# Kernel optimization log

Measured on AMD Instinct MI355X. Metric: run time of the kernel, lower is better.

## Reference

```python
import jax, jax.numpy as jnp
import numpy as np

HID = 64


def _rev_edges(row, col, n_nodes):
    # Find, for each directed edge (u,v), the index of its reverse (v,u).
    E = row.shape[0]
    keys = row.astype(jnp.int64) * n_nodes + col.astype(jnp.int64)
    rkeys = col.astype(jnp.int64) * n_nodes + row.astype(jnp.int64)
    order = jnp.argsort(keys)
    sk = keys[order]
    pos = jnp.clip(jnp.searchsorted(sk, rkeys), 0, E - 1)
    rev = order[pos]
    has_rev = sk[pos] == rkeys
    return rev, has_rev


def _dmpnn_conv(x, row, col, rev, has_rev, edge_hidden, Wm, bm, Wn, bn):
    # Original semantics: for edge i=(src,tgt), aggregate edge_hidden over all
    # edges j with row[j]==tgt, excluding the reverse edge (tgt,src).
    N = x.shape[0]
    seg = jax.ops.segment_sum(edge_hidden, row, num_segments=N)  # [N,H]
    msg_agg = seg[col] - jnp.where(has_rev[:, None], edge_hidden[rev], 0.0)  # [E,H]
    messages = jax.nn.relu(jnp.concatenate([x[row], msg_agg], axis=-1) @ Wm + bm)  # [E,H]
    node_msg = jax.ops.segment_sum(messages, col, num_segments=N)  # [N,H]
    x_out = jax.nn.relu(jnp.concatenate([x, node_msg], axis=-1) @ Wn + bn)  # [N,H]
    return x_out, messages


def setup_inputs() -> dict:
    key = jax.random.key(0)
    N, E2, B = 40000, 400000, 512  # nodes, undirected edges, graphs
    rng = np.random.default_rng(0)
    a = rng.integers(0, N, E2 * 3)
    b = rng.integers(0, N, E2 * 3)
    m = a != b
    a, b = a[m], b[m]
    canon = np.minimum(a, b).astype(np.int64) * N + np.maximum(a, b)
    _, uidx = np.unique(canon, return_index=True)
    uidx = np.sort(uidx)[:E2]
    a, b = a[uidx], b[uidx]
    row = np.concatenate([a, b]).astype(np.int32)
    col = np.concatenate([b, a]).astype(np.int32)
    edge_index = jnp.asarray(np.stack([row, col]))  # [2, 2*E2], every edge has a reverse
    E = edge_index.shape[1]
    batch = jnp.sort(jax.random.randint(jax.random.fold_in(key, 1), (N,), 0, B, dtype=jnp.int32))
    ks = jax.random.split(jax.random.fold_in(key, 2), 26)
    nrm = lambda k, s: jax.random.normal(k, s, dtype=jnp.float32)
    p = lambda k, s: nrm(k, s) * 0.05
    return {
        "x": nrm(ks[0], (N, 78)),
        "edge_attr": nrm(ks[1], (E, 6)),
        "xt": nrm(ks[2], (B, 128)),
        "edge_index": edge_index,
        "batch": batch,
        "n_graphs": B,
        "We": p(ks[3], (6, HID)), "be": p(ks[4], (HID,)),
        "Wm1": p(ks[5], (78 + HID, HID)), "bm1": p(ks[6], (HID,)),
        "Wn1": p(ks[7], (78 + HID, HID)), "bn1": p(ks[8], (HID,)),
        "Wm2": p(ks[9], (2 * HID, HID)), "bm2": p(ks[10], (HID,)),
        "Wn2": p(ks[11], (2 * HID, HID)), "bn2": p(ks[12], (HID,)),
        "Wm3": p(ks[13], (2 * HID, HID)), "bm3": p(ks[14], (HID,)),
        "Wn3": p(ks[15], (2 * HID, HID)), "bn3": p(ks[16], (HID,)),
        "Wxd": p(ks[17], (HID, 128)), "bxd": p(ks[18], (128,)),
        "W1": p(ks[19], (256, 1024)), "b1": p(ks[20], (1024,)),
        "W2": p(ks[21], (1024, 256)), "b2": p(ks[22], (256,)),
        "Wo": p(ks[23], (256, 1)), "bo": p(ks[24], (1,)),
    }


def reference(x, edge_attr, xt, edge_index, batch, n_graphs, We, be, Wm1, bm1, Wn1, bn1, Wm2, bm2, Wn2, bn2, Wm3, bm3, Wn3, bn3, Wxd, bxd, W1, b1, W2, b2, Wo, bo):
    N = x.shape[0]
    row, col = edge_index[0], edge_index[1]
    rev, has_rev = _rev_edges(row, col, N)
    eh = edge_attr @ We + be  # edge_init
    x1, eh = _dmpnn_conv(x, row, col, rev, has_rev, eh, Wm1, bm1, Wn1, bn1)
    x2, eh = _dmpnn_conv(x1, row, col, rev, has_rev, eh, Wm2, bm2, Wn2, bn2)
    x3, eh = _dmpnn_conv(x2, row, col, rev, has_rev, eh, Wm3, bm3, Wn3, bn3)
    pooled = jax.ops.segment_sum(x3, batch, num_segments=n_graphs)  # global_add_pool
    xg = jax.nn.relu(pooled @ Wxd + bxd)  # [B,128]
    xc = jnp.concatenate([xg, xt], axis=1)  # [B,256]
    h = jax.nn.relu(xc @ W1 + b1)
    h = jax.nn.relu(h @ W2 + b2)
    return h @ Wo + bo  # [B,1]
```

## Files before the change

### kernel.cpp

```cpp
#include <hip/hip_runtime.h>
#include <hip/hip_bf16.h>

using u16 = unsigned short;
using u32 = unsigned int;
using u64 = unsigned long long;

typedef short short8 __attribute__((ext_vector_type(8)));
typedef float f32x4 __attribute__((ext_vector_type(4)));

#define WP_TOP   0
#define WP_BOT   6144
#define WP_NTOP  10240
#define WP_NBOT  16384
#define WP_LAYER 20480

__device__ __forceinline__ float bf2f(u32 u){ union{u32 i; float f;} v; v.i = u<<16; return v.f; }
__device__ __forceinline__ u32 f2bf(float f){ union{float f; u32 i;} v; v.f=f; u32 i=v.i; return (i + 0x7FFFu + ((i>>16)&1u)) >> 16; }
__device__ __forceinline__ u32 pack2(float a, float b){ return f2bf(a) | (f2bf(b)<<16); }

__device__ __forceinline__ void store16bf(u16* d, const float* a){
  uint4 u0, u1;
  u0.x = pack2(a[0],a[1]);   u0.y = pack2(a[2],a[3]);
  u0.z = pack2(a[4],a[5]);   u0.w = pack2(a[6],a[7]);
  u1.x = pack2(a[8],a[9]);   u1.y = pack2(a[10],a[11]);
  u1.z = pack2(a[12],a[13]); u1.w = pack2(a[14],a[15]);
  *(uint4*)(d)   = u0;
  *(uint4*)(d+8) = u1;
}

__global__ __launch_bounds__(256) void k_deg(
    const int* __restrict__ row, int* __restrict__ cnt, int E)
{
  int e = blockIdx.x*256 + threadIdx.x;
  if (e >= E) return;
  atomicAdd(&cnt[row[e]], 1);
}

__global__ __launch_bounds__(256) void k_bsum(
    const int* __restrict__ cnt, int* __restrict__ bsum, int N)
{
  __shared__ int sh[256];
  int t = threadIdx.x;
  int i = blockIdx.x*256 + t;
  sh[t] = (i < N) ? cnt[i] : 0;
  __syncthreads();
  #pragma unroll
  for (int s=128; s; s>>=1){ if (t<s) sh[t]+=sh[t+s]; __syncthreads(); }
  if (t==0) bsum[blockIdx.x] = sh[0];
}

__global__ __launch_bounds__(256) void k_bscan(
    const int* __restrict__ bsum, int* __restrict__ bofs, int nb,
    int* __restrict__ off, int N)
{
  __shared__ int sh[256];
  int t = threadIdx.x;
  int v = (t < nb) ? bsum[t] : 0;
  sh[t] = v;
  __syncthreads();
  #pragma unroll
  for (int s=1; s<256; s<<=1){
    int u = (t>=s) ? sh[t-s] : 0;
    __syncthreads();
    sh[t] += u;
    __syncthreads();
  }
  if (t < nb) bofs[t] = sh[t] - v;
  if (t == 0) off[N] = sh[nb-1];
}

__global__ __launch_bounds__(256) void k_apply(
    const int* __restrict__ cnt, const int* __restrict__ bofs,
    int* __restrict__ off, int* __restrict__ nxt, int N)
{
  __shared__ int sh[256];
  int t = threadIdx.x;
  int i = blockIdx.x*256 + t;
  int v = (i < N) ? cnt[i] : 0;
  sh[t] = v;
  __syncthreads();
  #pragma unroll
  for (int s=1; s<256; s<<=1){
    int u = (t>=s) ? sh[t-s] : 0;
    __syncthreads();
    sh[t] += u;
    __syncthreads();
  }
  if (i < N){
    int ex = sh[t] - v + bofs[blockIdx.x];
    off[i] = ex;
    nxt[i] = ex;
  }
}

__global__ __launch_bounds__(256) void k_fill(
    const int* __restrict__ row, int* __restrict__ nxt,
    int* __restrict__ perm, int* __restrict__ iperm, int E)
{
  int e = blockIdx.x*256 + threadIdx.x;
  if (e >= E) return;
  int pos = atomicAdd(&nxt[row[e]], 1);
  perm[pos] = e;
  iperm[e] = pos;
}

__global__ __launch_bounds__(256) void k_permarr(
    const int* __restrict__ perm, const int* __restrict__ iperm,
    const int* __restrict__ row, const int* __restrict__ col,
    int* __restrict__ rowp, int* __restrict__ colp, int* __restrict__ revp,
    int E, int E2)
{
  int i = blockIdx.x*256 + threadIdx.x;
  if (i >= E) return;
  int e = perm[i];
  rowp[i] = row[e];
  colp[i] = col[e];
  int re = (e < E2) ? e + E2 : e - E2;
  revp[i] = iperm[re];
}

__global__ __launch_bounds__(256) void k_xconv(
    const float* __restrict__ x, u16* __restrict__ xbf, int N)
{
  int t = blockIdx.x*256 + threadIdx.x;
  if (t >= N*96) return;
  int n = t / 96, k = t - n*96;
  xbf[t] = (k < 78) ? (u16)f2bf(x[(size_t)n*78 + k]) : (u16)0;
}

__global__ __launch_bounds__(256) void k_edge_init(
    const float* __restrict__ ea, const int* __restrict__ perm,
    const float* __restrict__ We, const float* __restrict__ be,
    u16* __restrict__ eh, int E)
{
  int tid = blockIdx.x*256 + threadIdx.x;
  int i = tid >> 2;
  if (i >= E) return;
  int t = tid & 3;
  int e = perm[i];
  const float* a = ea + (size_t)e*6;
  float acc[16];
  #pragma unroll
  for (int j=0;j<16;j++) acc[j] = be[t*16+j];
  #pragma unroll
  for (int k=0;k<6;k++){
    float av = a[k];
    const float* w = We + k*64 + t*16;
    #pragma unroll
    for (int j=0;j<16;j++) acc[j] += av*w[j];
  }
  store16bf(eh + ((size_t)i<<6) + t*16, acc);
}

__global__ __launch_bounds__(256) void k_prepw(
    const float* __restrict__ Wm, const float* __restrict__ Wn,
    int XD, int KT, u16* __restrict__ dst)
{
  int t = blockIdx.x*256 + threadIdx.x;
  int topFL = KT*256;
  const float* W; int rbase, rvalid, dofs, fl;
  if (t < topFL)                   { W = Wm; rbase = 0;  rvalid = XD; dofs = WP_TOP;  fl = t; }
  else if (t < topFL+512)          { W = Wm; rbase = XD; rvalid = 64; dofs = WP_BOT;  fl = t - topFL; }
  else if (t < 2*topFL+512)        { W = Wn; rbase = 0;  rvalid = XD; dofs = WP_NTOP; fl = t - topFL - 512; }
  else if (t < 2*topFL+1024)       { W = Wn; rbase = XD; rvalid = 64; dofs = WP_NBOT; fl = t - 2*topFL - 512; }
  else return;
  int f = fl >> 6, lane = fl & 63;
  int nt = f & 3, kk = f >> 2;
  int n = (nt<<4) + (lane & 15);
  int krel = (kk<<5) + ((lane>>4)<<3);
  u16* d = dst + dofs + (size_t)f*512 + lane*8;
  #pragma unroll
  for (int j=0;j<8;j++){
    int kr = krel + j;
    d[j] = (kr < rvalid) ? (u16)f2bf(W[(size_t)(rbase+kr)*64 + n]) : (u16)0;
  }
}

__global__ __launch_bounds__(256) void k_packw(
    const float* __restrict__ W, int K, int Nout, u16* __restrict__ dst)
{
  int t = blockIdx.x*256 + threadIdx.x;
  int NT = Nout >> 4;
  int total = (K >> 5) * NT * 64;
  if (t >= total) return;
  int f = t >> 6, lane = t & 63;
  int nt = f % NT, kk = f / NT;
  int n = (nt<<4) + (lane & 15);
  int kb = (kk<<5) + ((lane>>4)<<3);
  u16* d = dst + ((size_t)f*64 + lane)*8;
  #pragma unroll
  for (int j=0;j<8;j++) d[j] = (u16)f2bf(W[(size_t)(kb+j)*Nout + n]);
}

__global__ __launch_bounds__(256) void k_gemm(
    const u16* __restrict__ A, int lda, const u16* __restrict__ BP,
    const float* __restrict__ bias, void* __restrict__ outv, int ldo,
    int M, int NT, int KT, int dorelu, int obf16)
{
  int lane = threadIdx.x & 63;
  int wid = (blockIdx.x << 2) + (threadIdx.x >> 6);
  int nb = NT >> 2;
  int mblk = wid / nb, nblk = wid - mblk*nb;
  int m0 = mblk << 4;
  if (m0 >= M) return;
  int n0 = nblk << 6;
  int nlo = lane & 15;
  int khi = (lane >> 4) << 3;
  int r0 = m0 + nlo; if (r0 > M-1) r0 = M-1;

  f32x4 acc[4];
  #pragma unroll
  for (int nt=0;nt<4;nt++){ f32x4 z = {0.f,0.f,0.f,0.f}; acc[nt]=z; }
  for (int kk=0; kk<KT; kk++){
    short8 a = *(const short8*)(A + (size_t)r0*lda + (kk<<5) + khi);
    #pragma unroll
    for (int nt=0;nt<4;nt++){
      short8 b = *(const short8*)(BP + ((size_t)(kk*NT + (nblk<<2) + nt)*64 + lane)*8);
      acc[nt] = __builtin_amdgcn_mfma_f32_16x16x32_bf16(a, b, acc[nt], 0,0,0);
    }
  }
  int mrow = (lane >> 4) << 2;
  #pragma unroll
  for (int r=0;r<4;r++){
    int m = m0 + mrow + r;
    if (m >= M) continue;
    #pragma unroll
    for (int nt=0;nt<4;nt++){
      float v = acc[nt][r] + bias[n0 + (nt<<4) + nlo];
      if (dorelu) v = fmaxf(v, 0.f);
      if (obf16) ((u16*)outv)[(size_t)m*ldo + n0 + (nt<<4) + nlo] = (u16)f2bf(v);
      else       ((float*)outv)[(size_t)m*ldo + n0 + (nt<<4) + nlo] = v;
    }
  }
}

__global__ __launch_bounds__(256) void k_seg(
    const u16* __restrict__ eh, const int* __restrict__ off,
    u16* __restrict__ segb, int N)
{
  int w = (blockIdx.x << 2) + (threadIdx.x >> 6);
  if (w >= N) return;
  int lane = threadIdx.x & 63;
  int lo = off[w], hi = off[w+1];
  float s = 0.f;
  for (int i = lo; i < hi; i++) s += bf2f((u32)eh[((size_t)i<<6) + lane]);
  segb[((size_t)w<<6) + lane] = (u16)f2bf(s);
}

template<int KT>
__global__ __launch_bounds__(256) void k_proj(
    const u16* __restrict__ xin, const u16* __restrict__ segb,
    const u16* __restrict__ wp, const float* __restrict__ bm,
    u16* __restrict__ pxb, u16* __restrict__ psb, int N)
{
  int lane = threadIdx.x & 63;
  int wid = (blockIdx.x << 2) + (threadIdx.x >> 6);
  int base = wid << 4;
  if (base >= N) return;
  int nlo = lane & 15;
  int khi = (lane >> 4) << 3;

  short8 bt[KT][4];
  #pragma unroll
  for (int kk=0;kk<KT;kk++)
    #pragma unroll
    for (int nt=0;nt<4;nt++)
      bt[kk][nt] = *(const short8*)(wp + WP_TOP + ((size_t)((kk<<2)|nt)*64 + lane)*8);
  short8 bb[2][4];
  #pragma unroll
  for (int kk=0;kk<2;kk++)
    #pragma unroll
    for (int nt=0;nt<4;nt++)
      bb[kk][nt] = *(const short8*)(wp + WP_BOT + ((size_t)((kk<<2)|nt)*64 + lane)*8);

  int r0 = base + nlo; if (r0 > N-1) r0 = N-1;
  const u16* xrow = xin + (size_t)r0*(KT*32);
  short8 ax[KT];
  #pragma unroll
  for (int kk=0;kk<KT;kk++) ax[kk] = *(const short8*)(xrow + (kk<<5) + khi);
  const u16* srow = segb + ((size_t)r0<<6);
  short8 as[2];
  #pragma unroll
  for (int kk=0;kk<2;kk++) as[kk] = *(const short8*)(srow + (kk<<5) + khi);

  f32x4 accP[4], accS[4];
  #pragma unroll
  for (int nt=0;nt<4;nt++){ f32x4 z = {0.f,0.f,0.f,0.f}; accP[nt]=z; accS[nt]=z; }
  #pragma unroll
  for (int kk=0;kk<KT;kk++)
    #pragma unroll
    for (int nt=0;nt<4;nt++)
      accP[nt] = __builtin_amdgcn_mfma_f32_16x16x32_bf16(ax[kk], bt[kk][nt], accP[nt], 0,0,0);
  #pragma unroll
  for (int kk=0;kk<2;kk++)
    #pragma unroll
    for (int nt=0;nt<4;nt++)
      accS[nt] = __builtin_amdgcn_mfma_f32_16x16x32_bf16(as[kk], bb[kk][nt], accS[nt], 0,0,0);

  float bmv[4];
  #pragma unroll
  for (int nt=0;nt<4;nt++) bmv[nt] = bm[(nt<<4) + nlo];

  int mrow = (lane >> 4) << 2;
  #pragma unroll
  for (int r=0;r<4;r++){
    int node = base + mrow + r;
    if (node >= N) continue;
    #pragma unroll
    for (int nt=0;nt<4;nt++){
      pxb[((size_t)node<<6) + (nt<<4) + nlo] = (u16)f2bf(accP[nt][r] + bmv[nt]);
      psb[((size_t)node<<6) + (nt<<4) + nlo] = (u16)f2bf(accS[nt][r]);
    }
  }
}

__global__ __launch_bounds__(256) void k_scatmfma(
    const u16* __restrict__ eh, const u16* __restrict__ wp,
    const u16* __restrict__ pxb, const u16* __restrict__ psb,
    const int* __restrict__ rowp, const int* __restrict__ colp,
    const int* __restrict__ revp, u16* __restrict__ msg, int E)
{
  int lane = threadIdx.x & 63;
  int wid = (blockIdx.x << 2) + (threadIdx.x >> 6);
  int base = wid << 4;
  if (base >= E) return;
  int nlo = lane & 15;
  int khi = (lane >> 4) << 3;

  short8 bb[2][4];
  #pragma unroll
  for (int kk=0;kk<2;kk++)
    #pragma unroll
    for (int nt=0;nt<4;nt++)
      bb[kk][nt] = *(const short8*)(wp + WP_BOT + ((size_t)((kk<<2)|nt)*64 + lane)*8);

  int sa = base + nlo; if (sa > E-1) sa = E-1;
  const u16* ehp = eh + ((size_t)sa<<6) + khi;
  short8 a0 = *(const short8*)(ehp);
  short8 a1 = *(const short8*)(ehp + 32);

  f32x4 acc[4];
  #pragma unroll
  for (int nt=0;nt<4;nt++){
    f32x4 z = {0.f,0.f,0.f,0.f};
    acc[nt] = z;
    acc[nt] = __builtin_amdgcn_mfma_f32_16x16x32_bf16(a0, bb[0][nt], acc[nt], 0,0,0);
    acc[nt] = __builtin_amdgcn_mfma_f32_16x16x32_bf16(a1, bb[1][nt], acc[nt], 0,0,0);
  }

  int mrow = (lane >> 4) << 2;
  #pragma unroll
  for (int r=0;r<4;r++){
    int slot = base + mrow + r;
    if (slot >= E) continue;
    int rp = rowp[slot];
    int cp = colp[slot];
    int rv = revp[slot];
    const u16* pr = psb + ((size_t)rp<<6) + nlo;
    const u16* pc = pxb + ((size_t)cp<<6) + nlo;
    u16* ob = msg + ((size_t)rv<<6) + nlo;
    #pragma unroll
    for (int nt=0;nt<4;nt++){
      float v = bf2f((u32)pc[nt<<4]) + bf2f((u32)pr[nt<<4]) - acc[nt][r];
      ob[nt<<4] = (u16)f2bf(fmaxf(v, 0.f));
    }
  }
}

__global__ __launch_bounds__(256) void k_gnmsg(
    const u16* __restrict__ msg, const int* __restrict__ revp,
    const int* __restrict__ off, u16* __restrict__ nmsgb,
    u16* __restrict__ segnext, int N)
{
  int w = (blockIdx.x << 2) + (threadIdx.x >> 6);
  if (w >= N) return;
  int lane = threadIdx.x & 63;
  int lo = off[w], hi = off[w+1];
  float s = 0.f, sg = 0.f;
  if (segnext) {
    for (int j = lo; j < hi; j++) {
      int i = revp[j];
      s  += bf2f((u32)msg[((size_t)i<<6) + lane]);
      sg += bf2f((u32)msg[((size_t)j<<6) + lane]);
    }
    segnext[((size_t)w<<6) + lane] = (u16)f2bf(sg);
  } else {
    for (int j = lo; j < hi; j++) {
      int i = revp[j];
      s += bf2f((u32)msg[((size_t)i<<6) + lane]);
    }
  }
  nmsgb[((size_t)w<<6) + lane] = (u16)f2bf(s);
}

template<int KT>
__global__ __launch_bounds__(256) void k_nodef(
    const u16* __restrict__ xin, const u16* __restrict__ nmsgb,
    const u16* __restrict__ wp, const float* __restrict__ bn,
    u16* __restrict__ xout, int N)
{
  int lane = threadIdx.x & 63;
  int wid = (blockIdx.x << 2) + (threadIdx.x >> 6);
  int base = wid << 4;
  if (base >= N) return;
  int nlo = lane & 15;
  int khi = (lane >> 4) << 3;

  short8 bt[KT][4];
  #pragma unroll
  for (int kk=0;kk<KT;kk++)
    #pragma unroll
    for (int nt=0;nt<4;nt++)
      bt[kk][nt] = *(const short8*)(wp + WP_NTOP + ((size_t)((kk<<2)|nt)*64 + lane)*8);
  short8 bb[2][4];
  #pragma unroll
  for (int kk=0;kk<2;kk++)
    #pragma unroll
    for (int nt=0;nt<4;nt++)
      bb[kk][nt] = *(const short8*)(wp + WP_NBOT + ((size_t)((kk<<2)|nt)*64 + lane)*8);

  int r0 = base + nlo; if (r0 > N-1) r0 = N-1;
  const u16* xrow = xin + (size_t)r0*(KT*32);
  short8 ax[KT];
  #pragma unroll
  for (int kk=0;kk<KT;kk++) ax[kk] = *(const short8*)(xrow + (kk<<5) + khi);
  const u16* mrp = nmsgb + ((size_t)r0<<6);
  short8 am[2];
  #pragma unroll
  for (int kk=0;kk<2;kk++) am[kk] = *(const short8*)(mrp + (kk<<5) + khi);

  f32x4 acc[4];
  #pragma unroll
  for (int nt=0;nt<4;nt++){ f32x4 z = {0.f,0.f,0.f,0.f}; acc[nt]=z; }
  #pragma unroll
  for (int kk=0;kk<KT;kk++)
    #pragma unroll
    for (int nt=0;nt<4;nt++)
      acc[nt] = __builtin_amdgcn_mfma_f32_16x16x32_bf16(ax[kk], bt[kk][nt], acc[nt], 0,0,0);
  #pragma unroll
  for (int kk=0;kk<2;kk++)
    #pragma unroll
    for (int nt=0;nt<4;nt++)
      acc[nt] = __builtin_amdgcn_mfma_f32_16x16x32_bf16(am[kk], bb[kk][nt], acc[nt], 0,0,0);

  float bnv[4];
  #pragma unroll
  for (int nt=0;nt<4;nt++) bnv[nt] = bn[(nt<<4) + nlo];

  int mrow = (lane >> 4) << 2;
  #pragma unroll
  for (int r=0;r<4;r++){
    int node = base + mrow + r;
    if (node >= N) continue;
    #pragma unroll
    for (int nt=0;nt<4;nt++)
      xout[((size_t)node<<6) + (nt<<4) + nlo] = (u16)f2bf(fmaxf(acc[nt][r] + bnv[nt], 0.f));
  }
}

__global__ __launch_bounds__(256) void k_goff(
    const int* __restrict__ batch, int* __restrict__ goff, int N, int B)
{
  int n = blockIdx.x*256 + threadIdx.x;
  if (n >= N) return;
  int bcur = batch[n];
  int bprev = (n == 0) ? -1 : batch[n-1];
  for (int g = bprev + 1; g <= bcur; ++g) goff[g] = n;
  if (n == N-1) { for (int g = bcur + 1; g <= B; ++g) goff[g] = N; }
}

__global__ __launch_bounds__(256) void k_pool(
    const u16* __restrict__ xin, const int* __restrict__ goff,
    u16* __restrict__ pooledb, int B)
{
  int g = (blockIdx.x << 2) + (threadIdx.x >> 6);
  if (g >= B) return;
  int lane = threadIdx.x & 63;
  int lo = goff[g], hi = goff[g + 1];
  float s = 0.f;
  for (int n = lo; n < hi; n++) s += bf2f((u32)xin[((size_t)n << 6) + lane]);
  pooledb[((size_t)g << 6) + lane] = (u16)f2bf(s);
}

__global__ __launch_bounds__(256) void k_xtconv(
    const float* __restrict__ xt, u16* __restrict__ ab1, int B)
{
  int t = blockIdx.x*256 + threadIdx.x;
  if (t >= B*128) return;
  int r = t >> 7, c = t & 127;
  ab1[(size_t)r*256 + 128 + c] = (u16)f2bf(xt[t]);
}

__global__ __launch_bounds__(256) void k_out(
    const float* __restrict__ h2, const float* __restrict__ Wo,
    const float* __restrict__ bo, float* __restrict__ out, int B)
{
  int w = (blockIdx.x << 2) + (threadIdx.x >> 6);
  if (w >= B) return;
  int lane = threadIdx.x & 63;
  const float* h = h2 + (size_t)w*256;
  float s = 0.f;
  #pragma unroll
  for (int k=0;k<4;k++) s += h[lane + (k<<6)] * Wo[lane + (k<<6)];
  #pragma unroll
  for (int off=32; off; off>>=1) s += __shfl_down(s, off, 64);
  if (lane == 0) out[w] = s + bo[0];
}

extern "C" void kernel_launch(void* const* d_in, const int* in_sizes, int n_in,
                              void* d_out, int out_size, void* d_ws, size_t ws_size,
                              hipStream_t stream)
{
  const float* x    = (const float*)d_in[0];
  const float* ea   = (const float*)d_in[1];
  const float* xt   = (const float*)d_in[2];
  const int*   eidx = (const int*)d_in[3];
  const int*   batch= (const int*)d_in[4];
  const float* We   = (const float*)d_in[6];
  const float* be   = (const float*)d_in[7];
  const float* Wm[3]= {(const float*)d_in[8],  (const float*)d_in[12], (const float*)d_in[16]};
  const float* bm[3]= {(const float*)d_in[9],  (const float*)d_in[13], (const float*)d_in[17]};
  const float* Wn[3]= {(const float*)d_in[10], (const float*)d_in[14], (const float*)d_in[18]};
  const float* bn[3]= {(const float*)d_in[11], (const float*)d_in[15], (const float*)d_in[19]};
  const float* Wxd  = (const float*)d_in[20];
  const float* bxd  = (const float*)d_in[21];
  const float* W1   = (const float*)d_in[22];
  const float* b1   = (const float*)d_in[23];
  const float* W2   = (const float*)d_in[24];
  const float* b2   = (const float*)d_in[25];
  const float* Wo   = (const float*)d_in[26];
  const float* bo   = (const float*)d_in[27];

  const int N = in_sizes[0] / 78;
  const int E = in_sizes[1] / 6;
  const int B = in_sizes[2] / 128;
  const int E2 = E / 2;
  const int* row = eidx;
  const int* col = eidx + E;

  char* p = (char*)d_ws;
  size_t off = 0;
  auto alloc = [&](size_t b)->void* {
    void* r = p + off;
    off = (off + b + 255) & ~(size_t)255;
    return r;
  };
  u16*   ehA   = (u16*)  alloc((size_t)E * 128);
  u16*   ehB   = (u16*)  alloc((size_t)E * 128);
  int*   rowp  = (int*)  alloc((size_t)E * 4);
  int*   colp  = (int*)  alloc((size_t)E * 4);
  int*   revp  = (int*)  alloc((size_t)E * 4);
  int*   offs  = (int*)  alloc((size_t)(N+1) * 4);
  u16*   xbf   = (u16*)  alloc((size_t)N * 192);
  u16*   sA    = (u16*)  alloc((size_t)N * 128);
  u16*   sB    = (u16*)  alloc((size_t)N * 128);
  u16*   pxb   = (u16*)  alloc((size_t)N * 128);
  u16*   psb   = (u16*)  alloc((size_t)N * 128);
  u16*   xa    = (u16*)  alloc((size_t)N * 128);
  u16*   xb    = (u16*)  alloc((size_t)N * 128);
  int*   goff  = (int*)  alloc((size_t)(B+1) * 4);
  u16*   pooledb=(u16*)  alloc((size_t)B * 128);
  u16*   ab1   = (u16*)  alloc((size_t)B * 512);
  u16*   h1b   = (u16*)  alloc((size_t)B * 2048);
  float* h2f   = (float*)alloc((size_t)B * 1024);
  u16*   wpack = (u16*)  alloc((size_t)3 * WP_LAYER * 2);
  u16*   wxdP  = (u16*)  alloc((size_t)(64/32)*(128/16)*512 * 2);
  u16*   w1P   = (u16*)  alloc((size_t)(256/32)*(1024/16)*512 * 2);
  u16*   w2P   = (u16*)  alloc((size_t)(1024/32)*(256/16)*512 * 2);

  char* ehBc = (char*)ehB;
  int* perm  = (int*)ehBc;
  int* iperm = perm + E;
  int* cnt   = iperm + E;
  int* nxt   = cnt + N;
  int* bsum  = nxt + N;
  int* bofs  = bsum + 1024;

  dim3 blk(256);
  int gE   = (E + 255) / 256;
  int gE4  = ((size_t)E*4 + 255) / 256;
  int gEm  = (E + 63) / 64;
  int gN   = (N + 255) / 256;
  int gNm  = (N + 63) / 64;
  int gNw  = (N + 3) / 4;
  int gBw  = (B + 3) / 4;
  int gXc  = (N*96 + 255) / 256;
  int nb   = (N + 255) / 256;

  hipMemsetAsync(cnt, 0, (size_t)N * 4, stream);
  k_deg  <<<gE, blk, 0, stream>>>(row, cnt, E);
  k_bsum <<<nb, blk, 0, stream>>>(cnt, bsum, N);
  k_bscan<<<1,  blk, 0, stream>>>(bsum, bofs, nb, offs, N);
  k_apply<<<nb, blk, 0, stream>>>(cnt, bofs, offs, nxt, N);
  k_fill <<<gE, blk, 0, stream>>>(row, nxt, perm, iperm, E);
  k_permarr<<<gE, blk, 0, stream>>>(perm, iperm, row, col, rowp, colp, revp, E, E2);
  k_edge_init<<<gE4, blk, 0, stream>>>(ea, perm, We, be, ehA, E);
  k_xconv<<<gXc, blk, 0, stream>>>(x, xbf, N);
  k_goff<<<gN, blk, 0, stream>>>(batch, goff, N, B);
  for (int L = 0; L < 3; ++L) {
    int XD = (L == 0) ? 78 : 64;
    int KT = (L == 0) ? 3 : 2;
    k_prepw<<<10, blk, 0, stream>>>(Wm[L], Wn[L], XD, KT, wpack + (size_t)L*WP_LAYER);
  }
  k_packw<<<(1024 + 255)/256, blk, 0, stream>>>(Wxd, 64, 128, wxdP);
  k_packw<<<(32768 + 255)/256, blk, 0, stream>>>(W1, 256, 1024, w1P);
  k_packw<<<(32768 + 255)/256, blk, 0, stream>>>(W2, 1024, 256, w2P);

  k_seg<<<gNw, blk, 0, stream>>>(ehA, offs, sA, N);

  const u16* ehin = ehA;
  u16* ehout = ehB;
  const u16* xin = xbf;
  u16* segcur = sA;
  u16* segnxt = sB;
  for (int L = 0; L < 3; ++L) {
    u16* xout = (L % 2 == 0) ? xa : xb;
    const u16* wp = wpack + (size_t)L*WP_LAYER;
    if (L == 0) k_proj<3><<<gNm, blk, 0, stream>>>(xin, segcur, wp, bm[L], pxb, psb, N);
    else        k_proj<2><<<gNm, blk, 0, stream>>>(xin, segcur, wp, bm[L], pxb, psb, N);
    k_scatmfma<<<gEm, blk, 0, stream>>>(ehin, wp, pxb, psb, rowp, colp, revp, ehout, E);
    k_gnmsg<<<gNw, blk, 0, stream>>>(ehout, revp, offs, pxb, (L < 2) ? segnxt : (u16*)nullptr, N);
    if (L == 0) k_nodef<3><<<gNm, blk, 0, stream>>>(xin, pxb, wp, bn[L], xout, N);
    else        k_nodef<2><<<gNm, blk, 0, stream>>>(xin, pxb, wp, bn[L], xout, N);
    u16* tmp = (u16*)ehin; ehin = ehout; ehout = tmp;
    u16* ts = segcur; segcur = segnxt; segnxt = ts;
    xin = xout;
  }

  k_pool<<<gBw, blk, 0, stream>>>(xa, goff, pooledb, B);
  k_xtconv<<<(B*128 + 255)/256, blk, 0, stream>>>(xt, ab1, B);
  {
    int waves = ((B + 15)/16) * (128/64);
    k_gemm<<<(waves + 3)/4, blk, 0, stream>>>(pooledb, 64, wxdP, bxd, ab1, 256, B, 128>>4, 64>>5, 1, 1);
  }
  {
    int waves = ((B + 15)/16) * (1024/64);
    k_gemm<<<(waves + 3)/4, blk, 0, stream>>>(ab1, 256, w1P, b1, h1b, 1024, B, 1024>>4, 256>>5, 1, 1);
  }
  {
    int waves = ((B + 15)/16) * (256/64);
    k_gemm<<<(waves + 3)/4, blk, 0, stream>>>(h1b, 1024, w2P, b2, h2f, 256, B, 256>>4, 1024>>5, 1, 0);
  }
  k_out<<<gBw, blk, 0, stream>>>(h2f, Wo, bo, (float*)d_out, B);
}
```

Measured before the change: 815.4 us.

## Switch to fp16, fold edge-init into first segment sum, vectorize gather

Moves all 16-bit storage and MFMA from bf16 to fp16, trading exponent range for cheaper hardware conversions and more mantissa. The edge-init kernel now iterates in original edge order and scatters into sorted slots. The first segment sum is computed algebraically from raw 6-wide edge attributes rather than re-reading the 64-wide hidden state. The per-node message gather uses four edge groups per wave with 8-byte loads and shuffle reductions to expose more memory parallelism.

```diff
diff --git a/kernel.cpp b/kernel.cpp
--- a/kernel.cpp
+++ b/kernel.cpp
@@ -1,5 +1,5 @@
 #include <hip/hip_runtime.h>
-#include <hip/hip_bf16.h>
+#include <hip/hip_fp16.h>
 
 using u16 = unsigned short;
 using u32 = unsigned int;
@@ -14,11 +14,11 @@
 #define WP_NBOT  16384
 #define WP_LAYER 20480
 
-__device__ __forceinline__ float bf2f(u32 u){ union{u32 i; float f;} v; v.i = u<<16; return v.f; }
-__device__ __forceinline__ u32 f2bf(float f){ union{float f; u32 i;} v; v.f=f; u32 i=v.i; return (i + 0x7FFFu + ((i>>16)&1u)) >> 16; }
-__device__ __forceinline__ u32 pack2(float a, float b){ return f2bf(a) | (f2bf(b)<<16); }
-
-__device__ __forceinline__ void store16bf(u16* d, const float* a){
+__device__ __forceinline__ float h2f(u16 u){ union{u16 s; _Float16 h;} v; v.s=u; return (float)v.h; }
+__device__ __forceinline__ u16 f2h(float f){ union{u16 s; _Float16 h;} v; v.h=(_Float16)f; return v.s; }
+__device__ __forceinline__ u32 pack2(float a, float b){ return (u32)f2h(a) | ((u32)f2h(b)<<16); }
+
+__device__ __forceinline__ void store16h(u16* d, const float* a){
   uint4 u0, u1;
   u0.x = pack2(a[0],a[1]);   u0.y = pack2(a[2],a[3]);
   u0.z = pack2(a[4],a[5]);   u0.w = pack2(a[6],a[7]);
@@ -120,24 +120,24 @@
 }
 
 __global__ __launch_bounds__(256) void k_xconv(
-    const float* __restrict__ x, u16* __restrict__ xbf, int N)
+    const float* __restrict__ x, u16* __restrict__ xh, int N)
 {
   int t = blockIdx.x*256 + threadIdx.x;
   if (t >= N*96) return;
   int n = t / 96, k = t - n*96;
-  xbf[t] = (k < 78) ? (u16)f2bf(x[(size_t)n*78 + k]) : (u16)0;
+  xh[t] = (k < 78) ? f2h(x[(size_t)n*78 + k]) : (u16)0;
 }
 
 __global__ __launch_bounds__(256) void k_edge_init(
-    const float* __restrict__ ea, const int* __restrict__ perm,
+    const float* __restrict__ ea, const int* __restrict__ iperm,
     const float* __restrict__ We, const float* __restrict__ be,
     u16* __restrict__ eh, int E)
 {
   int tid = blockIdx.x*256 + threadIdx.x;
-  int i = tid >> 2;
-  if (i >= E) return;
+  int e = tid >> 2;
+  if (e >= E) return;
   int t = tid & 3;
-  int e = perm[i];
+  int slot = iperm[e];
   const float* a = ea + (size_t)e*6;
   float acc[16];
   #pragma unroll
@@ -149,7 +149,32 @@
     #pragma unroll
     for (int j=0;j<16;j++) acc[j] += av*w[j];
   }
-  store16bf(eh + ((size_t)i<<6) + t*16, acc);
+  store16h(eh + ((size_t)slot<<6) + t*16, acc);
+}
+
+__global__ __launch_bounds__(256) void k_seg0(
+    const float* __restrict__ ea, const int* __restrict__ perm,
+    const int* __restrict__ off, const float* __restrict__ We,
+    const float* __restrict__ be, u16* __restrict__ segb, int N)
+{
+  int w = (blockIdx.x << 2) + (threadIdx.x >> 6);
+  if (w >= N) return;
+  int lane = threadIdx.x & 63;
+  int lo = off[w], hi = off[w+1];
+  float wcol[6];
+  #pragma unroll
+  for (int k=0;k<6;k++) wcol[k] = We[k*64 + lane];
+  float es[6] = {0.f,0.f,0.f,0.f,0.f,0.f};
+  for (int j = lo; j < hi; j++){
+    int e = perm[j];
+    const float* a = ea + (size_t)e*6;
+    #pragma unroll
+    for (int k=0;k<6;k++) es[k] += a[k];
+  }
+  float acc = (float)(hi - lo) * be[lane];
+  #pragma unroll
+  for (int k=0;k<6;k++) acc += es[k]*wcol[k];
+  segb[((size_t)w<<6) + lane] = f2h(acc);
 }
 
 __global__ __launch_bounds__(256) void k_prepw(
@@ -172,7 +197,7 @@
   #pragma unroll
   for (int j=0;j<8;j++){
     int kr = krel + j;
-    d[j] = (kr < rvalid) ? (u16)f2bf(W[(size_t)(rbase+kr)*64 + n]) : (u16)0;
+    d[j] = (kr < rvalid) ? f2h(W[(size_t)(rbase+kr)*64 + n]) : (u16)0;
   }
 }
 
@@ -189,13 +214,13 @@
   int kb = (kk<<5) + ((lane>>4)<<3);
   u16* d = dst + ((size_t)f*64 + lane)*8;
   #pragma unroll
-  for (int j=0;j<8;j++) d[j] = (u16)f2bf(W[(size_t)(kb+j)*Nout + n]);
+  for (int j=0;j<8;j++) d[j] = f2h(W[(size_t)(kb+j)*Nout + n]);
 }
 
 __global__ __launch_bounds__(256) void k_gemm(
     const u16* __restrict__ A, int lda, const u16* __restrict__ BP,
     const float* __restrict__ bias, void* __restrict__ outv, int ldo,
-    int M, int NT, int KT, int dorelu, int obf16)
+    int M, int NT, int KT, int dorelu, int oh16)
 {
   int lane = threadIdx.x & 63;
   int wid = (blockIdx.x << 2) + (threadIdx.x >> 6);
@@ -216,7 +241,7 @@
     #pragma unroll
     for (int nt=0;nt<4;nt++){
       short8 b = *(const short8*)(BP + ((size_t)(kk*NT + (nblk<<2) + nt)*64 + lane)*8);
-      acc[nt] = __builtin_amdgcn_mfma_f32_16x16x32_bf16(a, b, acc[nt], 0,0,0);
+      acc[nt] = __builtin_amdgcn_mfma_f32_16x16x32_f16(a, b, acc[nt], 0,0,0);
     }
   }
   int mrow = (lane >> 4) << 2;
@@ -228,23 +253,10 @@
     for (int nt=0;nt<4;nt++){
       float v = acc[nt][r] + bias[n0 + (nt<<4) + nlo];
       if (dorelu) v = fmaxf(v, 0.f);
-      if (obf16) ((u16*)outv)[(size_t)m*ldo + n0 + (nt<<4) + nlo] = (u16)f2bf(v);
-      else       ((float*)outv)[(size_t)m*ldo + n0 + (nt<<4) + nlo] = v;
+      if (oh16) ((u16*)outv)[(size_t)m*ldo + n0 + (nt<<4) + nlo] = f2h(v);
+      else      ((float*)outv)[(size_t)m*ldo + n0 + (nt<<4) + nlo] = v;
     }
   }
-}
-
-__global__ __launch_bounds__(256) void k_seg(
-    const u16* __restrict__ eh, const int* __restrict__ off,
-    u16* __restrict__ segb, int N)
-{
-  int w = (blockIdx.x << 2) + (threadIdx.x >> 6);
-  if (w >= N) return;
-  int lane = threadIdx.x & 63;
-  int lo = off[w], hi = off[w+1];
-  float s = 0.f;
-  for (int i = lo; i < hi; i++) s += bf2f((u32)eh[((size_t)i<<6) + lane]);
-  segb[((size_t)w<<6) + lane] = (u16)f2bf(s);
 }
 
 template<int KT>
@@ -290,12 +302,12 @@
   for (int kk=0;kk<KT;kk++)
     #pragma unroll
     for (int nt=0;nt<4;nt++)
-      accP[nt] = __builtin_amdgcn_mfma_f32_16x16x32_bf16(ax[kk], bt[kk][nt], accP[nt], 0,0,0);
+      accP[nt] = __builtin_amdgcn_mfma_f32_16x16x32_f16(ax[kk], bt[kk][nt], accP[nt], 0,0,0);
   #pragma unroll
   for (int kk=0;kk<2;kk++)
     #pragma unroll
     for (int nt=0;nt<4;nt++)
-      accS[nt] = __builtin_amdgcn_mfma_f32_16x16x32_bf16(as[kk], bb[kk][nt], accS[nt], 0,0,0);
+      accS[nt] = __builtin_amdgcn_mfma_f32_16x16x32_f16(as[kk], bb[kk][nt], accS[nt], 0,0,0);
 
   float bmv[4];
   #pragma unroll
@@ -308,8 +320,8 @@
     if (node >= N) continue;
     #pragma unroll
     for (int nt=0;nt<4;nt++){
-      pxb[((size_t)node<<6) + (nt<<4) + nlo] = (u16)f2bf(accP[nt][r] + bmv[nt]);
-      psb[((size_t)node<<6) + (nt<<4) + nlo] = (u16)f2bf(accS[nt][r]);
+      pxb[((size_t)node<<6) + (nt<<4) + nlo] = f2h(accP[nt][r] + bmv[nt]);
+      psb[((size_t)node<<6) + (nt<<4) + nlo] = f2h(accS[nt][r]);
     }
   }
 }
@@ -344,8 +356,8 @@
   for (int nt=0;nt<4;nt++){
     f32x4 z = {0.f,0.f,0.f,0.f};
     acc[nt] = z;
-    acc[nt] = __builtin_amdgcn_mfma_f32_16x16x32_bf16(a0, bb[0][nt], acc[nt], 0,0,0);
-    acc[nt] = __builtin_amdgcn_mfma_f32_16x16x32_bf16(a1, bb[1][nt], acc[nt], 0,0,0);
+    acc[nt] = __builtin_amdgcn_mfma_f32_16x16x32_f16(a0, bb[0][nt], acc[nt], 0,0,0);
+    acc[nt] = __builtin_amdgcn_mfma_f32_16x16x32_f16(a1, bb[1][nt], acc[nt], 0,0,0);
   }
 
   int mrow = (lane >> 4) << 2;
@@ -361,8 +373,8 @@
     u16* ob = msg + ((size_t)rv<<6) + nlo;
     #pragma unroll
     for (int nt=0;nt<4;nt++){
-      float v = bf2f((u32)pc[nt<<4]) + bf2f((u32)pr[nt<<4]) - acc[nt][r];
-      ob[nt<<4] = (u16)f2bf(fmaxf(v, 0.f));
+      float v = h2f(pc[nt<<4]) + h2f(pr[nt<<4]) - acc[nt][r];
+      ob[nt<<4] = f2h(fmaxf(v, 0.f));
     }
   }
 }
@@ -375,22 +387,43 @@
   int w = (blockIdx.x << 2) + (threadIdx.x >> 6);
   if (w >= N) return;
   int lane = threadIdx.x & 63;
+  int g = lane >> 4, l = lane & 15;
   int lo = off[w], hi = off[w+1];
-  float s = 0.f, sg = 0.f;
-  if (segnext) {
-    for (int j = lo; j < hi; j++) {
+  float s0=0.f,s1=0.f,s2=0.f,s3=0.f;
+  float t0=0.f,t1=0.f,t2=0.f,t3=0.f;
+  if (segnext){
+    for (int j = lo + g; j < hi; j += 4){
       int i = revp[j];
-      s  += bf2f((u32)msg[((size_t)i<<6) + lane]);
-      sg += bf2f((u32)msg[((size_t)j<<6) + lane]);
+      uint2 v = *(const uint2*)(msg + ((size_t)i<<6) + (l<<2));
+      uint2 u = *(const uint2*)(msg + ((size_t)j<<6) + (l<<2));
+      s0 += h2f((u16)v.x); s1 += h2f((u16)(v.x>>16)); s2 += h2f((u16)v.y); s3 += h2f((u16)(v.y>>16));
+      t0 += h2f((u16)u.x); t1 += h2f((u16)(u.x>>16)); t2 += h2f((u16)u.y); t3 += h2f((u16)(u.y>>16));
     }
-    segnext[((size_t)w<<6) + lane] = (u16)f2bf(sg);
   } else {
-    for (int j = lo; j < hi; j++) {
+    for (int j = lo + g; j < hi; j += 4){
       int i = revp[j];
-      s += bf2f((u32)msg[((size_t)i<<6) + lane]);
+      uint2 v = *(const uint2*)(msg + ((size_t)i<<6) + (l<<2));
+      s0 += h2f((u16)v.x); s1 += h2f((u16)(v.x>>16)); s2 += h2f((u16)v.y); s3 += h2f((u16)(v.y>>16));
     }
   }
-  nmsgb[((size_t)w<<6) + lane] = (u16)f2bf(s);
+  s0 += __shfl_xor(s0,16,64); s0 += __shfl_xor(s0,32,64);
+  s1 += __shfl_xor(s1,16,64); s1 += __shfl_xor(s1,32,64);
+  s2 += __shfl_xor(s2,16,64); s2 += __shfl_xor(s2,32,64);
+  s3 += __shfl_xor(s3,16,64); s3 += __shfl_xor(s3,32,64);
+  if (segnext){
+    t0 += __shfl_xor(t0,16,64); t0 += __shfl_xor(t0,32,64);
+    t1 += __shfl_xor(t1,16,64); t1 += __shfl_xor(t1,32,64);
+    t2 += __shfl_xor(t2,16,64); t2 += __shfl_xor(t2,32,64);
+    t3 += __shfl_xor(t3,16,64); t3 += __shfl_xor(t3,32,64);
+  }
+  if (g == 0){
+    uint2 o; o.x = pack2(s0,s1); o.y = pack2(s2,s3);
+    *(uint2*)(nmsgb + ((size_t)w<<6) + (l<<2)) = o;
+    if (segnext){
+      uint2 q; q.x = pack2(t0,t1); q.y = pack2(t2,t3);
+      *(uint2*)(segnext + ((size_t)w<<6) + (l<<2)) = q;
+    }
+  }
 }
 
 template<int KT>
@@ -436,12 +469,12 @@
   for (int kk=0;kk<KT;kk++)
     #pragma unroll
     for (int nt=0;nt<4;nt++)
-      acc[nt] = __builtin_amdgcn_mfma_f32_16x16x32_bf16(ax[kk], bt[kk][nt], acc[nt], 0,0,0);
+      acc[nt] = __builtin_amdgcn_mfma_f32_16x16x32_f16(ax[kk], bt[kk][nt], acc[nt], 0,0,0);
   #pragma unroll
   for (int kk=0;kk<2;kk++)
     #pragma unroll
     for (int nt=0;nt<4;nt++)
-      acc[nt] = __builtin_amdgcn_mfma_f32_16x16x32_bf16(am[kk], bb[kk][nt], acc[nt], 0,0,0);
+      acc[nt] = __builtin_amdgcn_mfma_f32_16x16x32_f16(am[kk], bb[kk][nt], acc[nt], 0,0,0);
 
   float bnv[4];
   #pragma unroll
@@ -454,7 +487,7 @@
     if (node >= N) continue;
     #pragma unroll
     for (int nt=0;nt<4;nt++)
-      xout[((size_t)node<<6) + (nt<<4) + nlo] = (u16)f2bf(fmaxf(acc[nt][r] + bnv[nt], 0.f));
+      xout[((size_t)node<<6) + (nt<<4) + nlo] = f2h(fmaxf(acc[nt][r] + bnv[nt], 0.f));
   }
 }
 
@@ -471,15 +504,15 @@
 
 __global__ __launch_bounds__(256) void k_pool(
     const u16* __restrict__ xin, const int* __restrict__ goff,
-    u16* __restrict__ pooledb, int B)
+    u16* __restrict__ pooledh, int B)
 {
   int g = (blockIdx.x << 2) + (threadIdx.x >> 6);
   if (g >= B) return;
   int lane = threadIdx.x & 63;
   int lo = goff[g], hi = goff[g + 1];
   float s = 0.f;
-  for (int n = lo; n < hi; n++) s += bf2f((u32)xin[((size_t)n << 6) + lane]);
-  pooledb[((size_t)g << 6) + lane] = (u16)f2bf(s);
+  for (int n = lo; n < hi; n++) s += h2f(xin[((size_t)n << 6) + lane]);
+  pooledh[((size_t)g << 6) + lane] = f2h(s);
 }
 
 __global__ __launch_bounds__(256) void k_xtconv(
@@ -488,7 +521,7 @@
   int t = blockIdx.x*256 + threadIdx.x;
   if (t >= B*128) return;
   int r = t >> 7, c = t & 127;
-  ab1[(size_t)r*256 + 128 + c] = (u16)f2bf(xt[t]);
+  ab1[(size_t)r*256 + 128 + c] = f2h(xt[t]);
 }
 
 __global__ __launch_bounds__(256) void k_out(
@@ -551,7 +584,7 @@
   int*   colp  = (int*)  alloc((size_t)E * 4);
   int*   revp  = (int*)  alloc((size_t)E * 4);
   int*   offs  = (int*)  alloc((size_t)(N+1) * 4);
-  u16*   xbf   = (u16*)  alloc((size_t)N * 192);
+  u16*   xh    = (u16*)  alloc((size_t)N * 192);
   u16*   sA    = (u16*)  alloc((size_t)N * 128);
   u16*   sB    = (u16*)  alloc((size_t)N * 128);
   u16*   pxb   = (u16*)  alloc((size_t)N * 128);
@@ -559,9 +592,9 @@
   u16*   xa    = (u16*)  alloc((size_t)N * 128);
   u16*   xb    = (u16*)  alloc((size_t)N * 128);
   int*   goff  = (int*)  alloc((size_t)(B+1) * 4);
-  u16*   pooledb=(u16*)  alloc((size_t)B * 128);
+  u16*   pooledh=(u16*)  alloc((size_t)B * 128);
   u16*   ab1   = (u16*)  alloc((size_t)B * 512);
-  u16*   h1b   = (u16*)  alloc((size_t)B * 2048);
+  u16*   h1h   = (u16*)  alloc((size_t)B * 2048);
   float* h2f   = (float*)alloc((size_t)B * 1024);
   u16*   wpack = (u16*)  alloc((size_t)3 * WP_LAYER * 2);
   u16*   wxdP  = (u16*)  alloc((size_t)(64/32)*(128/16)*512 * 2);
@@ -594,8 +627,9 @@
   k_apply<<<nb, blk, 0, stream>>>(cnt, bofs, offs, nxt, N);
   k_fill <<<gE, blk, 0, stream>>>(row, nxt, perm, iperm, E);
   k_permarr<<<gE, blk, 0, stream>>>(perm, iperm, row, col, rowp, colp, revp, E, E2);
-  k_edge_init<<<gE4, blk, 0, stream>>>(ea, perm, We, be, ehA, E);
-  k_xconv<<<gXc, blk, 0, stream>>>(x, xbf, N);
+  k_edge_init<<<gE4, blk, 0, stream>>>(ea, iperm, We, be, ehA, E);
+  k_seg0<<<gNw, blk, 0, stream>>>(ea, perm, offs, We, be, sA, N);
+  k_xconv<<<gXc, blk, 0, stream>>>(x, xh, N);
   k_goff<<<gN, blk, 0, stream>>>(batch, goff, N, B);
   for (int L = 0; L < 3; ++L) {
     int XD = (L == 0) ? 78 : 64;
@@ -606,11 +640,9 @@
   k_packw<<<(32768 + 255)/256, blk, 0, stream>>>(W1, 256, 1024, w1P);
   k_packw<<<(32768 + 255)/256, blk, 0, stream>>>(W2, 1024, 256, w2P);
 
-  k_seg<<<gNw, blk, 0, stream>>>(ehA, offs, sA, N);
-
   const u16* ehin = ehA;
   u16* ehout = ehB;
-  const u16* xin = xbf;
+  const u16* xin = xh;
   u16* segcur = sA;
   u16* segnxt = sB;
   for (int L = 0; L < 3; ++L) {
@@ -627,19 +659,19 @@
     xin = xout;
   }
 
-  k_pool<<<gBw, blk, 0, stream>>>(xa, goff, pooledb, B);
+  k_pool<<<gBw, blk, 0, stream>>>(xa, goff, pooledh, B);
   k_xtconv<<<(B*128 + 255)/256, blk, 0, stream>>>(xt, ab1, B);
   {
     int waves = ((B + 15)/16) * (128/64);
-    k_gemm<<<(waves + 3)/4, blk, 0, stream>>>(pooledb, 64, wxdP, bxd, ab1, 256, B, 128>>4, 64>>5, 1, 1);
+    k_gemm<<<(waves + 3)/4, blk, 0, stream>>>(pooledh, 64, wxdP, bxd, ab1, 256, B, 128>>4, 64>>5, 1, 1);
   }
   {
     int waves = ((B + 15)/16) * (1024/64);
-    k_gemm<<<(waves + 3)/4, blk, 0, stream>>>(ab1, 256, w1P, b1, h1b, 1024, B, 1024>>4, 256>>5, 1, 1);
+    k_gemm<<<(waves + 3)/4, blk, 0, stream>>>(ab1, 256, w1P, b1, h1h, 1024, B, 1024>>4, 256>>5, 1, 1);
   }
   {
     int waves = ((B + 15)/16) * (256/64);
-    k_gemm<<<(waves + 3)/4, blk, 0, stream>>>(h1b, 1024, w2P, b2, h2f, 256, B, 256>>4, 1024>>5, 1, 0);
+    k_gemm<<<(waves + 3)/4, blk, 0, stream>>>(h1h, 1024, w2P, b2, h2f, 256, B, 256>>4, 1024>>5, 1, 0);
   }
   k_out<<<gBw, blk, 0, stream>>>(h2f, Wo, bo, (float*)d_out, B);
 }
```

After: 728.9 us. -10.6%, faster.
